# Kernel optimization log

Hardware: AMD Instinct MI355X
Metric: run time of the kernel (lower is better)

## Reference

```python
import jax, jax.numpy as jnp
import numpy as np

LMAX=4; MMAX=2; L2=25; M2=19; C=64; CE=64; NRBF=600; CUT=5.0
HEADS=8; ACH=32; VCH=16; HMSG=64; HFF=128; G=288; NL=2
AVG_NEI=20.0; AVG_NODES=2000.0
N_NODES=2000; N_EDGES=40000; NSPEC=90
# |m| group of each truncated (edge-frame) coefficient, order l=0..4, m=-min(l,2)..min(l,2)
MG = np.array([0, 1,0,1, 2,1,0,1,2, 2,1,0,1,2, 2,1,0,1,2])
# l of each full SH coefficient (25 total)
LOC = np.array([0] + [1]*3 + [2]*5 + [3]*7 + [4]*9)

def silu(x):
    return x * jax.nn.sigmoid(x)

def rms_norm_sh(x, w):
    # x: [N, 25, C]; w: [5, C] per-degree affine weight (rms_norm_sh)
    ms = jnp.mean(x * x, axis=1, keepdims=True)
    return x * jax.lax.rsqrt(ms + 1e-6) * w[LOC][None]

def setup_inputs() -> dict:
    key = jax.random.key(0)
    ks = iter(jax.random.split(key, 64))
    def rn(shape, scale):
        return jax.random.normal(next(ks), shape, dtype=jnp.float32) * scale
    inp = {}
    inp['edge_vectors'] = rn((N_EDGES, 3), 1.5)
    inp['wigner'] = rn((N_EDGES, M2, L2), 0.2)
    inp['wigner_inv'] = rn((N_EDGES, L2, M2), 0.2)
    inp['species_embed'] = rn((NSPEC, C), 1.0)
    inp['edge_species_embed'] = rn((NSPEC, 2 * CE), 1.0)
    DIN = NRBF + 2 * CE  # 728
    inp['deg_W1'] = rn((DIN, 128), DIN ** -0.5)
    inp['deg_b1'] = jnp.zeros((128,), jnp.float32)
    inp['deg_W2'] = rn((128, M2 * C), 128 ** -0.5)
    inp['deg_b2'] = jnp.zeros((M2 * C,), jnp.float32)
    inp['norm1_w'] = jnp.ones((NL, 5, C), jnp.float32)
    inp['rad_W1'] = rn((NL, DIN, 128), DIN ** -0.5)
    inp['rad_b1'] = jnp.zeros((NL, 128), jnp.float32)
    inp['rad_W2'] = rn((NL, 128, 3 * 2 * C), 128 ** -0.5)
    inp['rad_b2'] = jnp.ones((NL, 3 * 2 * C), jnp.float32)
    inp['so2_W'] = rn((NL, 3, 2 * C, HMSG), (2 * C) ** -0.5)
    inp['alpha_W'] = rn((NL, HMSG, HEADS * ACH), HMSG ** -0.5)
    inp['alpha_vec'] = rn((NL, HEADS, ACH), ACH ** -0.5)
    inp['value_W'] = rn((NL, 3, HMSG, HEADS * VCH), HMSG ** -0.5)
    inp['proj_W'] = rn((NL, 3, HEADS * VCH, C), (HEADS * VCH) ** -0.5)
    inp['norm2_w'] = jnp.ones((NL, 5, C), jnp.float32)
    inp['ffn_W1'] = rn((NL, C, HFF), C ** -0.5)
    inp['ffn_b1'] = jnp.zeros((NL, HFF), jnp.float32)
    inp['ffn_W2'] = rn((NL, HFF, C), HFF ** -0.5)
    inp['to_grid'] = rn((G, L2), L2 ** -0.5)
    inp['from_grid'] = rn((L2, G), G ** -0.5)
    inp['final_norm_w'] = jnp.ones((5, C), jnp.float32)
    inp['en_W1'] = rn((C, HFF), C ** -0.5)
    inp['en_b1'] = jnp.zeros((HFF,), jnp.float32)
    inp['en_W2'] = rn((HFF, 1), HFF ** -0.5)
    inp['en_b2'] = jnp.zeros((1,), jnp.float32)
    inp['node_species'] = jax.random.randint(next(ks), (N_NODES,), 0, NSPEC, dtype=jnp.int32)
    inp['senders'] = jax.random.randint(next(ks), (N_EDGES,), 0, N_NODES, dtype=jnp.int32)
    inp['receivers'] = jax.random.randint(next(ks), (N_EDGES,), 0, N_NODES, dtype=jnp.int32)
    inp['n_node'] = jnp.array([N_NODES], jnp.int32)
    return inp

def reference(edge_vectors, wigner, wigner_inv, species_embed, edge_species_embed,
              deg_W1, deg_b1, deg_W2, deg_b2, norm1_w, rad_W1, rad_b1, rad_W2, rad_b2,
              so2_W, alpha_W, alpha_vec, value_W, proj_W, norm2_w, ffn_W1, ffn_b1, ffn_W2,
              to_grid, from_grid, final_norm_w, en_W1, en_b1, en_W2, en_b2,
              node_species, senders, receivers, n_node):
    N = node_species.shape[0]
    E = senders.shape[0]
    mg = jnp.asarray(MG)
    # Gaussian RBF distance expansion (rbf_width=2.0)
    d = jnp.sqrt(jnp.sum(edge_vectors * edge_vectors, axis=-1) + 1e-12)
    offs = jnp.linspace(0.0, CUT, NRBF)
    std = 2.0 * (CUT / (NRBF - 1))
    rbf = jnp.exp(-0.5 * ((d[:, None] - offs[None, :]) / std) ** 2)  # [E, 600]
    # shared atom-edge embedding concat
    ne = edge_species_embed[node_species]
    se, re = jnp.split(ne, 2, axis=-1)
    ee = jnp.concatenate([rbf, se[senders], re[receivers]], axis=1)  # [E, 728]
    # initial node features: species embedding on l=0 component
    x = jnp.zeros((N, L2, C), dtype=edge_vectors.dtype).at[:, 0, :].set(species_embed[node_species])
    # edge degree embedding: radial MLP -> edge-frame coeffs -> rotate back -> scatter
    h = silu(ee @ deg_W1 + deg_b1) @ deg_W2 + deg_b2
    deg = jnp.einsum('elm,emc->elc', wigner_inv, h.reshape(E, M2, C))  # [E,25,C]
    x = x + jax.ops.segment_sum(deg, receivers, num_segments=N) / AVG_NEI
    for i in range(NL):
        # --- SO2 equivariant graph attention ---
        res = x
        xn = rms_norm_sh(x, norm1_w[i])
        msg = jnp.concatenate([xn[senders], xn[receivers]], axis=-1)      # [E,25,2C]
        msg = jnp.einsum('eml,elc->emc', wigner, msg)                     # rotate to edge frame [E,19,2C]
        rad = (silu(ee @ rad_W1[i] + rad_b1[i]) @ rad_W2[i] + rad_b2[i]).reshape(E, MMAX + 1, 2 * C)
        msg = msg * rad[:, mg]                                            # per-|m| radial modulation
        h = jnp.einsum('emc,mco->emo', msg, so2_W[i][mg])                 # SO2 conv [E,19,HMSG]
        a = (silu(h[:, 0, :]) @ alpha_W[i]).reshape(E, HEADS, ACH)        # invariant (m=0) alpha path
        logits = jnp.sum(silu(a) * alpha_vec[i][None], axis=-1)           # [E,HEADS]
        mx = jax.ops.segment_max(logits, receivers, num_segments=N)[receivers]
        ex = jnp.exp(logits - mx)
        den = jax.ops.segment_sum(ex, receivers, num_segments=N)[receivers]
        attn = ex / (den + 1e-12)
        v = jnp.einsum('emo,mov->emv', h, value_W[i][mg]).reshape(E, M2, HEADS, VCH)
        v = (v * attn[:, None, :, None]).reshape(E, M2, HEADS * VCH)
        oe = jnp.einsum('emv,mvc->emc', v, proj_W[i][mg])                 # [E,19,C]
        oe = jnp.einsum('elm,emc->elc', wigner_inv, oe)                   # rotate back [E,25,C]
        x = res + jax.ops.segment_sum(oe, receivers, num_segments=N)
        # --- S2 grid feed-forward ---
        res = x
        xn = rms_norm_sh(x, norm2_w[i])
        g = jnp.einsum('gl,nlc->ngc', to_grid, xn)                        # [N,288,C]
        g = silu(g @ ffn_W1[i] + ffn_b1[i]) @ ffn_W2[i]
        x = res + jnp.einsum('lg,ngc->nlc', from_grid, g)
    # final norm + energy head
    xn = rms_norm_sh(x, final_norm_w)
    g = jnp.einsum('gl,nlc->ngc', to_grid, xn)
    g = silu(g @ en_W1 + en_b1) @ en_W2 + en_b2
    eo = jnp.einsum('lg,ngo->nlo', from_grid, g)
    return eo[:, 0, 0] / AVG_NODES
```

## Files before the change

### kernel.cpp

```cpp
#include <hip/hip_runtime.h>
#include <hip/hip_bf16.h>
#include <math.h>


#define NRBF 600
#define DIN 728
#define GPTS 288
#define CH 8

typedef __attribute__((ext_vector_type(8))) short bf16x8;
typedef __attribute__((ext_vector_type(4))) float f32x4;

__constant__ int d_mg[19] = {0,1,0,1,2,1,0,1,2,2,1,0,1,2,2,1,0,1,2};
__constant__ int d_loc[25] = {0,1,1,1,2,2,2,2,2,3,3,3,3,3,3,3,4,4,4,4,4,4,4,4,4};
__constant__ int d_mg0[5]={0,2,6,11,16};
__constant__ int d_mg1[8]={1,3,5,7,10,12,15,17};
__constant__ int d_mg2[6]={4,8,9,13,14,18};

__device__ inline float silu_f(float v){ return v/(1.0f+__expf(-v)); }
__device__ inline float bf2f(unsigned short u){ return __uint_as_float(((unsigned)u)<<16); }
__device__ inline unsigned short f2bf(float f){
  unsigned b=__float_as_uint(f);
  return (unsigned short)((b + 0x7FFF + ((b>>16)&1)) >> 16);
}

__device__ inline void atomicMaxF(float* addr, float val){
  int* ia=(int*)addr;
  int old=*ia;
  while (__int_as_float(old) < val){
    int assumed=old;
    old = atomicCAS(ia, assumed, __float_as_int(val));
    if (old == assumed) break;
  }
}

__global__ __launch_bounds__(256) void zero_cnt_kernel(int* cnt, int N){
  int i = blockIdx.x*256+threadIdx.x;
  if (i<N) cnt[i]=0;
}
__global__ __launch_bounds__(256) void csr_count_kernel(const int* __restrict__ rcv, int* cnt, int E){
  int i = blockIdx.x*256+threadIdx.x;
  if (i<E) atomicAdd(&cnt[rcv[i]],1);
}
__global__ __launch_bounds__(256) void csr_scan_kernel(const int* __restrict__ cnt,
    int* rowptr, int* fill, int N){
  __shared__ int s_part[256];
  int tid=threadIdx.x;
  int chunk=(N+255)/256;
  int lvals[12];
  int base=tid*chunk;
  int lsum=0;
  for (int i=0;i<chunk && i<12;i++){
    int v=(base+i<N)?cnt[base+i]:0;
    lvals[i]=lsum; lsum+=v;
  }
  s_part[tid]=lsum;
  __syncthreads();
  if (tid==0){
    int run=0;
    for (int t=0;t<256;t++){ int v=s_part[t]; s_part[t]=run; run+=v; }
  }
  __syncthreads();
  int off=s_part[tid];
  for (int i=0;i<chunk && i<12;i++){
    if (base+i<N){ rowptr[base+i]=off+lvals[i]; fill[base+i]=off+lvals[i]; }
  }
  if (tid==255) rowptr[N]=off+lsum;
}
__global__ __launch_bounds__(256) void csr_fill_kernel(const int* __restrict__ rcv,
    int* fill, int* eix, int E){
  int i = blockIdx.x*256+threadIdx.x;
  if (i<E){ int p=atomicAdd(&fill[rcv[i]],1); eix[p]=i; }
}

__global__ __launch_bounds__(256) void wsvb_kernel(const float* __restrict__ so2W,
    const float* __restrict__ valW, unsigned short* __restrict__ wsvb){
  int i=blockIdx.x/3, g=blockIdx.x%3;
  const float* A = so2W + (size_t)i*24576 + g*8192;
  const float* B = valW + (size_t)i*24576 + g*8192;
  unsigned short* C = wsvb + (size_t)blockIdx.x*16384;
  __shared__ float sB[8192];
  for (int j=threadIdx.x;j<2048;j+=256) ((float4*)sB)[j]=((const float4*)B)[j];
  __syncthreads();
  for (int idx=threadIdx.x; idx<16384; idx+=256){
    int k=idx>>7, j=idx&127;
    float acc=0;
    #pragma unroll 4
    for (int o=0;o<64;o++) acc += A[k*64+o]*sB[o*128+j];
    int pos = ((k>>5)*8 + (j>>4))*512 + (((k>>3)&3)*16 + (j&15))*8 + (k&7);
    C[pos]=f2bf(acc);
  }
}

__global__ __launch_bounds__(256) void projb_kernel(const float* __restrict__ pW,
    unsigned short* __restrict__ projb){
  const float* src = pW + (size_t)blockIdx.x*8192;
  unsigned short* dst = projb + (size_t)blockIdx.x*8192;
  for (int idx=threadIdx.x; idx<8192; idx+=256){
    int k=idx>>6, j=idx&63;
    int pos = ((k>>5)*4 + (j>>4))*512 + (((k>>3)&3)*16 + (j&15))*8 + (k&7);
    dst[pos]=f2bf(src[idx]);
  }
}

__global__ __launch_bounds__(256) void packB2g_kernel(const float* __restrict__ src,
    unsigned short* __restrict__ dh, unsigned short* __restrict__ dl, int K, int Nn){
  int ktiles=(K+31)>>5;
  int nnt=Nn>>4;
  int tot=ktiles*nnt*512;
  for (int idx=blockIdx.x*256+threadIdx.x; idx<tot; idx+=gridDim.x*256){
    int f=idx>>9, r=idx&511, lane=r>>3, j=r&7;
    int kt=f/nnt, nt=f-kt*nnt;
    int k=kt*32+(lane>>4)*8+j, c=nt*16+(lane&15);
    float v=(k<K)? src[k*Nn+c] : 0.0f;
    unsigned short h=f2bf(v);
    dh[idx]=h;
    dl[idx]=f2bf(v-bf2f(h));
  }
}

__global__ __launch_bounds__(256) void pack_tg2_kernel(const float* __restrict__ tg,
    unsigned short* __restrict__ tgp){
  int tid=threadIdx.x;
  for (int idx=tid; idx<9216; idx+=256){
    int t=idx>>9, r=idx&511, lane=r>>3, j=r&7;
    int kl=(lane>>4)*8+j, row=t*16+(lane&15);
    float v=(kl<25)? tg[row*25+kl] : 0.0f;
    unsigned short h=f2bf(v);
    tgp[idx]=h;
    tgp[9216+idx]=f2bf(v-bf2f(h));
  }
}

__global__ __launch_bounds__(256) void pack_fg2_kernel(const float* __restrict__ fg,
    unsigned short* __restrict__ fgp){
  int tid=threadIdx.x;
  for (int idx=tid; idx<18432; idx+=256){
    int f=idx>>9, r=idx&511, lane=r>>3, j=r&7;
    int t=f>>1, mt=f&1;
    int row=mt*16+(lane&15), k=(lane>>4)*8+j;
    float v=(row<25 && k<16)? fg[row*288+t*16+k] : 0.0f;
    unsigned short h=f2bf(v);
    fgp[idx]=h;
    fgp[18432+idx]=f2bf(v-bf2f(h));
  }
}

__global__ __launch_bounds__(256) void mlpf_kernel(const float* __restrict__ ev,
    const float* __restrict__ ese, const int* __restrict__ nsp,
    const unsigned short* __restrict__ dw1h, const unsigned short* __restrict__ dw1l,
    const float* __restrict__ db1,
    const unsigned short* __restrict__ dw2h, const unsigned short* __restrict__ dw2l,
    const float* __restrict__ db2,
    const unsigned short* __restrict__ r1h, const unsigned short* __restrict__ r1l,
    const float* __restrict__ rb1,
    const unsigned short* __restrict__ r2h, const unsigned short* __restrict__ r2l,
    const float* __restrict__ rb2,
    const int* __restrict__ snd, const int* __restrict__ rcv, const int* __restrict__ eix,
    int do_deg,
    unsigned short* __restrict__ degout, float* __restrict__ radout, int E){
  int tid=threadIdx.x, wv=tid>>6, lane=tid&63;
  int lanelo=lane&15, khi=lane>>4;
  int p0=blockIdx.x*16;
  __shared__ unsigned short s_eeh[4096], s_eel[4096];
  __shared__ unsigned short s_h1h[2048], s_h1l[2048];
  __shared__ float s_d[16]; __shared__ int s_ss[16], s_rs[16], s_e[16];
  if (tid<16){
    int p=p0+tid;
    int e=(p<E)? eix[p] : -1;
    s_e[tid]=e;
    if (e>=0){
      float vx=ev[3*e], vy=ev[3*e+1], vz=ev[3*e+2];
      s_d[tid]=sqrtf(vx*vx+vy*vy+vz*vz+1e-12f);
      s_ss[tid]=nsp[snd[e]]; s_rs[tid]=nsp[rcv[e]];
    } else { s_d[tid]=0.0f; s_ss[tid]=0; s_rs[tid]=0; }
  }
  __syncthreads();
  const float step=5.0f/599.0f, inv_std=1.0f/(2.0f*step);
  int nta=wv*2, ntb=nta+1;
  f32x4 z4={0,0,0,0};
  f32x4 aD0=z4,aD1=z4,aR0=z4,aR1=z4;
  for (int c=0;c<23;c+=CH){
    int ncur=23-c; if (ncur>CH) ncur=CH;
    for (int idx=tid; idx<ncur*512; idx+=256){
      int f=idx>>9, r=idx&511, ln=r>>3, j=r&7;
      int k=(c+f)*32+((ln>>4)<<3)+j, row=ln&15;
      float v=0.0f;
      if (k<NRBF){ float t=(s_d[row]-k*step)*inv_std; v=__expf(-0.5f*t*t); }
      else if (k<NRBF+64) v=ese[s_ss[row]*128+(k-NRBF)];
      else if (k<DIN)     v=ese[s_rs[row]*128+64+(k-NRBF-64)];
      unsigned short h=f2bf(v);
      s_eeh[idx]=h; s_eel[idx]=f2bf(v-bf2f(h));
    }
    __syncthreads();
    for (int f=0; f<ncur; f++){
      int kt=c+f;
      bf16x8 Ah=*(const bf16x8*)(s_eeh + f*512 + lane*8);
      bf16x8 Al=*(const bf16x8*)(s_eel + f*512 + lane*8);
      size_t ba=(size_t)(kt*8+nta)*512+lane*8;
      {
        bf16x8 Bh=*(const bf16x8*)(r1h+ba), Bl=*(const bf16x8*)(r1l+ba);
        bf16x8 Bh2=*(const bf16x8*)(r1h+ba+512), Bl2=*(const bf16x8*)(r1l+ba+512);
        aR0=__builtin_amdgcn_mfma_f32_16x16x32_bf16(Ah,Bh,aR0,0,0,0);
        aR0=__builtin_amdgcn_mfma_f32_16x16x32_bf16(Al,Bh,aR0,0,0,0);
        aR0=__builtin_amdgcn_mfma_f32_16x16x32_bf16(Ah,Bl,aR0,0,0,0);
        aR1=__builtin_amdgcn_mfma_f32_16x16x32_bf16(Ah,Bh2,aR1,0,0,0);
        aR1=__builtin_amdgcn_mfma_f32_16x16x32_bf16(Al,Bh2,aR1,0,0,0);
        aR1=__builtin_amdgcn_mfma_f32_16x16x32_bf16(Ah,Bl2,aR1,0,0,0);
      }
      if (do_deg){
        bf16x8 Bh=*(const bf16x8*)(dw1h+ba), Bl=*(const bf16x8*)(dw1l+ba);
        bf16x8 Bh2=*(const bf16x8*)(dw1h+ba+512), Bl2=*(const bf16x8*)(dw1l+ba+512);
        aD0=__builtin_amdgcn_mfma_f32_16x16x32_bf16(Ah,Bh,aD0,0,0,0);
        aD0=__builtin_amdgcn_mfma_f32_16x16x32_bf16(Al,Bh,aD0,0,0,0);
        aD0=__builtin_amdgcn_mfma_f32_16x16x32_bf16(Ah,Bl,aD0,0,0,0);
        aD1=__builtin_amdgcn_mfma_f32_16x16x32_bf16(Ah,Bh2,aD1,0,0,0);
        aD1=__builtin_amdgcn_mfma_f32_16x16x32_bf16(Al,Bh2,aD1,0,0,0);
        aD1=__builtin_amdgcn_mfma_f32_16x16x32_bf16(Ah,Bl2,aD1,0,0,0);
      }
    }
    __syncthreads();
  }
  int nmlp = do_deg ? 2 : 1;
  #pragma unroll 1
  for (int it=0; it<nmlp; it++){
    int is_deg = (it==1);
    f32x4 a0 = is_deg ? aD0 : aR0;
    f32x4 a1 = is_deg ? aD1 : aR1;
    const float* b1 = is_deg ? db1 : rb1;
    #pragma unroll
    for (int q=0;q<4;q++){
      int row=khi*4+q;
      {
        int col=nta*16+lanelo;
        float v=silu_f(a0[q]+b1[col]);
        int pos=row*128 + (((col>>3)^(row&7))<<3) + (col&7);
        unsigned short h=f2bf(v);
        s_h1h[pos]=h; s_h1l[pos]=f2bf(v-bf2f(h));
      }
      {
        int col=ntb*16+lanelo;
        float v=silu_f(a1[q]+b1[col]);
        int pos=row*128 + (((col>>3)^(row&7))<<3) + (col&7);
        unsigned short h=f2bf(v);
        s_h1h[pos]=h; s_h1l[pos]=f2bf(v-bf2f(h));
      }
    }
    __syncthreads();
    bf16x8 Ahh[4],Ahl[4];
    #pragma unroll
    for (int kt=0;kt<4;kt++){
      int o=lanelo*128 + (((kt*4+khi)^(lanelo&7))<<3);
      Ahh[kt]=*(const bf16x8*)(s_h1h+o);
      Ahl[kt]=*(const bf16x8*)(s_h1l+o);
    }
    __syncthreads();
    if (is_deg){
      for (int nt=wv; nt<76; nt+=4){
        f32x4 acc=z4;
        #pragma unroll
        for (int kt=0;kt<4;kt++){
          size_t bo=(size_t)(kt*76+nt)*512+lane*8;
          bf16x8 Bh=*(const bf16x8*)(dw2h+bo), Bl=*(const bf16x8*)(dw2l+bo);
          acc=__builtin_amdgcn_mfma_f32_16x16x32_bf16(Ahh[kt],Bh,acc,0,0,0);
          acc=__builtin_amdgcn_mfma_f32_16x16x32_bf16(Ahl[kt],Bh,acc,0,0,0);
          acc=__builtin_amdgcn_mfma_f32_16x16x32_bf16(Ahh[kt],Bl,acc,0,0,0);
        }
        int col=nt*16+lanelo;
        float bb=db2[col];
        #pragma unroll
        for (int q=0;q<4;q++){
          int p=p0+khi*4+q;
          if (p<E) degout[(size_t)p*1216+col]=f2bf(acc[q]+bb);
        }
      }
    } else {
      for (int nt=wv; nt<24; nt+=4){
        f32x4 acc=z4;
        #pragma unroll
        for (int kt=0;kt<4;kt++){
          size_t bo=(size_t)(kt*24+nt)*512+lane*8;
          bf16x8 Bh=*(const bf16x8*)(r2h+bo), Bl=*(const bf16x8*)(r2l+bo);
          acc=__builtin_amdgcn_mfma_f32_16x16x32_bf16(Ahh[kt],Bh,acc,0,0,0);
          acc=__builtin_amdgcn_mfma_f32_16x16x32_bf16(Ahl[kt],Bh,acc,0,0,0);
          acc=__builtin_amdgcn_mfma_f32_16x16x32_bf16(Ahh[kt],Bl,acc,0,0,0);
        }
        int col=nt*16+lanelo;
        float bb=rb2[col];
        #pragma unroll
        for (int q=0;q<4;q++){
          int e=s_e[khi*4+q];
          if (e>=0) radout[(size_t)e*384+col]=acc[q]+bb;
        }
      }
    }
  }
}

__global__ __launch_bounds__(256) void node_sum_kernel(const unsigned short* __restrict__ msgb,
    const float* __restrict__ winv, const int* __restrict__ rowptr, const int* __restrict__ eix,
    const int* __restrict__ nsp, const float* __restrict__ spe,
    float* __restrict__ x, int mode, int N){
  int n=blockIdx.x, tid=threadIdx.x, wv=tid>>6, lane=tid&63;
  __shared__ float s_winv[4][480];
  __shared__ unsigned short s_oe[4][1216];
  __shared__ float4 s_red[4][400];
  int row0=rowptr[n];
  int cnt=rowptr[n+1]-row0;
  float4 acc[7];
  #pragma unroll
  for (int t=0;t<7;t++) acc[t]=make_float4(0,0,0,0);
  for (int j=wv; j<cnt; j+=4){
    int p=row0+j;
    int e=eix[p];
    asm volatile("s_waitcnt lgkmcnt(0)" ::: "memory");
    for (int k=lane;k<475;k+=64) s_winv[wv][k]=winv[(size_t)e*475+k];
    if (mode==1){
      for (int k=lane;k<152;k+=64)
        ((int4*)s_oe[wv])[k]=*(const int4*)(msgb+(size_t)p*1216+k*8);
    } else {
      for (int k=lane;k<152;k+=64){
        int m=k>>3, jj=k&7;
        ((int4*)s_oe[wv])[k]=*(const int4*)(msgb+(size_t)p*2432+m*128+jj*8);
      }
    }
    asm volatile("s_waitcnt lgkmcnt(0)" ::: "memory");
    const unsigned* o2=(const unsigned*)s_oe[wv];
    #pragma unroll
    for (int t=0;t<7;t++){
      int sI=lane+t*64;
      if (sI<400){
        int l=sI>>4, c4=sI&15;
        const float* wr=s_winv[wv]+l*19;
        float4 a=acc[t];
        #pragma unroll
        for (int m=0;m<19;m++){
          float w=wr[m];
          unsigned ua=o2[m*32+c4*2], ub=o2[m*32+c4*2+1];
          a.x+=w*bf2f((unsigned short)(ua&0xffffu));
          a.y+=w*bf2f((unsigned short)(ua>>16));
          a.z+=w*bf2f((unsigned short)(ub&0xffffu));
          a.w+=w*bf2f((unsigned short)(ub>>16));
        }
        acc[t]=a;
      }
    }
  }
  asm volatile("s_waitcnt lgkmcnt(0)" ::: "memory");
  #pragma unroll
  for (int t=0;t<7;t++){
    int sI=lane+t*64;
    if (sI<400) s_red[wv][sI]=acc[t];
  }
  __syncthreads();
  float4* xp=(float4*)(x+(size_t)n*1600);
  if (mode==0){
    for (int j=tid;j<400;j+=256){
      float4 a=s_red[0][j], b=s_red[1][j], c=s_red[2][j], d=s_red[3][j];
      float4 cur=xp[j];
      cur.x+=a.x+b.x+c.x+d.x;
      cur.y+=a.y+b.y+c.y+d.y;
      cur.z+=a.z+b.z+c.z+d.z;
      cur.w+=a.w+b.w+c.w+d.w;
      xp[j]=cur;
    }
  } else {
    int sp=nsp[n];
    const float4* sp4=(const float4*)(spe+(size_t)sp*64);
    for (int j=tid;j<400;j+=256){
      int l=j>>4, c4=j&15;
      float4 a=s_red[0][j], b=s_red[1][j], c=s_red[2][j], d=s_red[3][j];
      float4 base=(l==0)? sp4[c4] : make_float4(0,0,0,0);
      float4 o;
      o.x=base.x+0.05f*(a.x+b.x+c.x+d.x);
      o.y=base.y+0.05f*(a.y+b.y+c.y+d.y);
      o.z=base.z+0.05f*(a.z+b.z+c.z+d.z);
      o.w=base.w+0.05f*(a.w+b.w+c.w+d.w);
      xp[j]=o;
    }
  }
}

__global__ __launch_bounds__(256) void rmsnorm_kernel(const float* __restrict__ x,
    const float* __restrict__ w, float* __restrict__ xn, int N){
  int n = blockIdx.x, tid = threadIdx.x;
  __shared__ float s_x[1600];
  __shared__ float s_part[256];
  __shared__ float s_ms[64];
  const float* xr = x + (size_t)n*1600;
  for (int j=tid;j<1600;j+=256) s_x[j]=xr[j];
  __syncthreads();
  {
    int c = tid&63, seg = tid>>6;
    float acc=0;
    for (int l=seg;l<25;l+=4){ float v=s_x[l*64+c]; acc+=v*v; }
    s_part[tid]=acc;
  }
  __syncthreads();
  if (tid<64){
    float m=(s_part[tid]+s_part[tid+64]+s_part[tid+128]+s_part[tid+192])*(1.0f/25.0f);
    s_ms[tid]=rsqrtf(m+1e-6f);
  }
  __syncthreads();
  float* xo = xn + (size_t)n*1600;
  for (int j=tid;j<1600;j+=256){
    int l=j>>6, c=j&63;
    xo[j]=s_x[j]*s_ms[c]*w[d_loc[l]*64+c];
  }
}

__global__ __launch_bounds__(256) void init_mxden_kernel(float* mx, float* den, int N){
  int idx = blockIdx.x*256+threadIdx.x;
  if (idx < N*8){ mx[idx]=-3.0e38f; den[idx]=0.0f; }
}

__global__ __launch_bounds__(256) void logits_kernel(const float* __restrict__ xn,
    const float* __restrict__ wig, const float* __restrict__ radb,
    const float* __restrict__ so2W, const float* __restrict__ alphaW, const float* __restrict__ alphaV,
    const int* __restrict__ snd, const int* __restrict__ rcv,
    float* __restrict__ logits, float* __restrict__ mx, int E){
  int e = blockIdx.x, tid = threadIdx.x;
  __shared__ float s_cat[3200];
  __shared__ float s_wig0[25];
  __shared__ float s_msg0[128];
  __shared__ float s_sh0[64];
  __shared__ float s_a[256];
  int s = snd[e], r = rcv[e];
  const float4* xs4 = (const float4*)(xn + (size_t)s*1600);
  const float4* xr4 = (const float4*)(xn + (size_t)r*1600);
  float4* cat4 = (float4*)s_cat;
  for (int j=tid;j<400;j+=256){
    int l=j>>4, c4=j&15;
    cat4[l*32+c4]    = xs4[j];
    cat4[l*32+16+c4] = xr4[j];
  }
  if (tid<25) s_wig0[tid]=wig[(size_t)e*475+tid];
  __syncthreads();
  if (tid<128){
    float acc=0;
    #pragma unroll
    for (int l=0;l<25;l++) acc += s_wig0[l]*s_cat[l*128+tid];
    s_msg0[tid]=acc*radb[(size_t)e*384+tid];
  }
  __syncthreads();
  if (tid<64){
    float acc=0;
    #pragma unroll
    for (int k=0;k<128;k++) acc += s_msg0[k]*so2W[k*64+tid];
    s_sh0[tid]=silu_f(acc);
  }
  __syncthreads();
  {
    float acc=0;
    #pragma unroll
    for (int o=0;o<64;o++) acc += s_sh0[o]*alphaW[o*256+tid];
    s_a[tid]=silu_f(acc)*alphaV[tid];
  }
  __syncthreads();
  if (tid<8){
    float lg=0;
    #pragma unroll
    for (int q=0;q<32;q++) lg += s_a[tid*32+q];
    logits[(size_t)e*8+tid]=lg;
    atomicMaxF(&mx[r*8+tid], lg);
  }
}

__global__ __launch_bounds__(256) void den_kernel(const float* __restrict__ logits,
    const float* __restrict__ mx, const int* __restrict__ rcv,
    float* __restrict__ den, int E){
  int idx = blockIdx.x*256+threadIdx.x;
  if (idx >= E*8) return;
  int e = idx>>3, hd = idx&7, r = rcv[e];
  atomicAdd(&den[r*8+hd], __expf(logits[idx]-mx[r*8+hd]));
}

__global__ __launch_bounds__(256) void msg_kernel(const float* __restrict__ xn,
    const float* __restrict__ wig, const float* __restrict__ radb,
    const int* __restrict__ snd, const int* __restrict__ rcv, const int* __restrict__ eix,
    unsigned short* __restrict__ msgb, int E){
  __shared__ float s_wig[1900];
  int tid=threadIdx.x, wv=tid>>6, lane=tid&63;
  int p=blockIdx.x*4+wv;
  bool act=(p<E);
  int pc=act? p : (E-1);
  int e=eix[pc];
  int node=(lane<32)? snd[e] : rcv[e];
  int c2=(lane&31)*2;
  int col0=c2+((lane>>5)<<6);
  const float* xb=xn+(size_t)node*1600+c2;
  float ca[25], cb[25];
  #pragma unroll
  for (int l=0;l<25;l++){
    float2 v=*(const float2*)(xb+l*64);
    ca[l]=v.x; cb[l]=v.y;
  }
  float* swig=s_wig+wv*475;
  for (int j=lane;j<475;j+=64) swig[j]=wig[(size_t)e*475+j];
  float ra0,ra1,rb0,rb1,rc0,rc1;
  {
    const float* rb_=radb+(size_t)e*384;
    float2 v0=*(const float2*)(rb_+col0);
    float2 v1=*(const float2*)(rb_+128+col0);
    float2 v2=*(const float2*)(rb_+256+col0);
    ra0=v0.x; ra1=v0.y; rb0=v1.x; rb1=v1.y; rc0=v2.x; rc1=v2.y;
  }
  __syncthreads();
  unsigned short* dst=msgb+(size_t)pc*2432+col0;
  constexpr int mgc[19]={0,1,0,1,2,1,0,1,2,2,1,0,1,2,2,1,0,1,2};
  if (act){
    #pragma unroll
    for (int m=0;m<19;m++){
      float a0=0.0f,a1=0.0f;
      const float* wr=swig+m*25;
      #pragma unroll
      for (int l=0;l<25;l++){ float w=wr[l]; a0+=w*ca[l]; a1+=w*cb[l]; }
      float r0,r1;
      if (mgc[m]==0){ r0=ra0; r1=ra1; }
      else if (mgc[m]==1){ r0=rb0; r1=rb1; }
      else { r0=rc0; r1=rc1; }
      a0*=r0; a1*=r1;
      unsigned packv=((unsigned)f2bf(a1)<<16)|(unsigned)f2bf(a0);
      *(unsigned*)(dst+m*128)=packv;
    }
  }
}

__global__ __launch_bounds__(256) void attn_gemm_kernel(unsigned short* __restrict__ msgb,
    const unsigned short* __restrict__ wsvp, const unsigned short* __restrict__ projp,
    const float* __restrict__ logits, const float* __restrict__ mx, const float* __restrict__ den,
    const int* __restrict__ eix, const int* __restrict__ rcv, int E){
  int tid=threadIdx.x, wv=tid>>6, lane=tid&63;
  int lanelo=lane&15, khi=lane>>4;
  int p0=blockIdx.x*16;
  __shared__ unsigned short s_vv[2176];
  __shared__ float s_attn[16][8];
  __shared__ short s_r2e[304], s_r2m[304];
  for (int j=tid;j<304;j+=256){
    int e,m;
    if (j<80){ e=j/5; m=d_mg0[j%5]; }
    else if (j<208){ int q=j-80; e=q>>3; m=d_mg1[q&7]; }
    else { int q=j-208; e=q/6; m=d_mg2[q%6]; }
    s_r2e[j]=(short)e; s_r2m[j]=(short)m;
  }
  if (tid<128){
    int i=tid>>3, h=tid&7, p=p0+i;
    float a=0.0f;
    if (p<E){
      int e=eix[p]; int r=rcv[e];
      a=__expf(logits[(size_t)e*8+h]-mx[r*8+h])/(den[r*8+h]+1e-12f);
    }
    s_attn[i][h]=a;
  }
  __syncthreads();
  const int4* wp4=(const int4*)wsvp;
  const int4* pp4=(const int4*)projp;
  for (int t=0;t<19;t++){
    int g=(t<5)?0:((t<13)?1:2);
    int R=t*16+lanelo;
    int ei=s_r2e[R], mi=s_r2m[R];
    int pp=p0+ei;
    size_t abase=((size_t)((pp<E)?pp:0))*2432 + (size_t)mi*128;
    bf16x8 A[4];
    #pragma unroll
    for (int kt=0;kt<4;kt++)
      A[kt]=*(const bf16x8*)(msgb + abase + kt*32 + khi*8);
    #pragma unroll
    for (int h2=0;h2<2;h2++){
      int nt=wv*2+h2;
      f32x4 acc={0,0,0,0};
      #pragma unroll
      for (int kt=0;kt<4;kt++){
        int4 tt=wp4[g*2048+(kt*8+nt)*64+lane];
        acc=__builtin_amdgcn_mfma_f32_16x16x32_bf16(A[kt],*(bf16x8*)&tt,acc,0,0,0);
      }
      int col=nt*16+lanelo;
      #pragma unroll
      for (int q=0;q<4;q++){
        int r16=khi*4+q;
        int ei2=s_r2e[t*16+r16];
        s_vv[r16*136+col]=f2bf(acc[q]*s_attn[ei2][nt]);
      }
    }
    __syncthreads();
    {
      bf16x8 A2[4];
      #pragma unroll
      for (int kt=0;kt<4;kt++)
        A2[kt]=*(const bf16x8*)(s_vv + lanelo*136 + kt*32 + khi*8);
      f32x4 acc={0,0,0,0};
      #pragma unroll
      for (int kt=0;kt<4;kt++){
        int4 tt=pp4[g*1024+(kt*4+wv)*64+lane];
        acc=__builtin_amdgcn_mfma_f32_16x16x32_bf16(A2[kt],*(bf16x8*)&tt,acc,0,0,0);
      }
      int col=wv*16+lanelo;
      #pragma unroll
      for (int q=0;q<4;q++){
        int R2=t*16+khi*4+q;
        int pi=p0+s_r2e[R2];
        if (pi<E) msgb[(size_t)pi*2432 + (size_t)s_r2m[R2]*128 + col]=f2bf(acc[q]);
      }
    }
    __syncthreads();
  }
}

__global__ __launch_bounds__(256) void grid_ffn_mfma_kernel(const float* __restrict__ xn,
    const unsigned short* __restrict__ tgp, const unsigned short* __restrict__ fgp,
    const unsigned short* __restrict__ w1p, const unsigned short* __restrict__ w2p,
    const float* __restrict__ b1, float* __restrict__ x, int N){
  int n=blockIdx.x, tid=threadIdx.x, wv=tid>>6, lane=tid&63;
  int lanelo=lane&15, khi=lane>>4;
  __shared__ __align__(16) char s_mem[74240];
  unsigned short* s_w1=(unsigned short*)s_mem;
  unsigned short* s_xn=(unsigned short*)(s_mem+32768);
  float* s_b1=(float*)(s_mem+40960);
  unsigned short* scr=(unsigned short*)(s_mem+41472)+(size_t)wv*4096;
  for (int j=tid;j<2048;j+=256) ((int4*)s_w1)[j]=((const int4*)w1p)[j];
  if (tid<128) s_b1[tid]=b1[tid];
  { int4 z={0,0,0,0}; for (int j=tid;j<512;j+=256) ((int4*)s_xn)[j]=z; }
  __syncthreads();
  {
    const float* xr=xn+(size_t)n*1600;
    for (int j=tid;j<1600;j+=256){
      int k=j>>6, c=j&63;
      float v=xr[j];
      unsigned short h=f2bf(v);
      s_xn[c*32+k]=h;
      s_xn[2048+c*32+k]=f2bf(v-bf2f(h));
    }
  }
  __syncthreads();
  bf16x8 XBh[4],XBl[4];
  #pragma unroll
  for (int ct=0;ct<4;ct++){
    int o=(ct*16+lanelo)*32 + khi*8;
    XBh[ct]=*(const bf16x8*)(s_xn+o);
    XBl[ct]=*(const bf16x8*)(s_xn+2048+o);
  }
  f32x4 oacc[2][4];
  #pragma unroll
  for (int mt=0;mt<2;mt++)
    #pragma unroll
    for (int nt=0;nt<4;nt++){ f32x4 z={0,0,0,0}; oacc[mt][nt]=z; }
  for (int t=wv;t<18;t+=4){
    bf16x8 Atgh=*(const bf16x8*)(tgp + t*512 + lane*8);
    bf16x8 Atgl=*(const bf16x8*)(tgp + 9216 + t*512 + lane*8);
    #pragma unroll
    for (int ct=0;ct<4;ct++){
      f32x4 g={0,0,0,0};
      g=__builtin_amdgcn_mfma_f32_16x16x32_bf16(Atgh,XBh[ct],g,0,0,0);
      g=__builtin_amdgcn_mfma_f32_16x16x32_bf16(Atgl,XBh[ct],g,0,0,0);
      g=__builtin_amdgcn_mfma_f32_16x16x32_bf16(Atgh,XBl[ct],g,0,0,0);
      #pragma unroll
      for (int q=0;q<4;q++){
        int row=khi*4+q, col=ct*16+lanelo;
        int pos=row*64 + (((col>>3)^(row&7))<<3) + (col&7);
        float v=g[q]; unsigned short h=f2bf(v);
        scr[pos]=h; scr[1024+pos]=f2bf(v-bf2f(h));
      }
    }
    bf16x8 Agh[2],Agl[2];
    #pragma unroll
    for (int kt=0;kt<2;kt++){
      int o=lanelo*64 + (((kt*4+khi)^(lanelo&7))<<3);
      Agh[kt]=*(const bf16x8*)(scr+o);
      Agl[kt]=*(const bf16x8*)(scr+1024+o);
    }
    #pragma unroll
    for (int nt=0;nt<8;nt++){
      f32x4 h={0,0,0,0};
      #pragma unroll
      for (int kt=0;kt<2;kt++){
        bf16x8 Bh=*(const bf16x8*)(s_w1 + (kt*8+nt)*512 + lane*8);
        bf16x8 Bl=*(const bf16x8*)(s_w1 + 8192 + (kt*8+nt)*512 + lane*8);
        h=__builtin_amdgcn_mfma_f32_16x16x32_bf16(Agh[kt],Bh,h,0,0,0);
        h=__builtin_amdgcn_mfma_f32_16x16x32_bf16(Agl[kt],Bh,h,0,0,0);
        h=__builtin_amdgcn_mfma_f32_16x16x32_bf16(Agh[kt],Bl,h,0,0,0);
      }
      #pragma unroll
      for (int q=0;q<4;q++){
        int row=khi*4+q, col=nt*16+lanelo;
        float v=silu_f(h[q]+s_b1[col]);
        int pos=row*128 + (((col>>3)^(row&7))<<3) + (col&7);
        unsigned short hh=f2bf(v);
        scr[pos]=hh; scr[2048+pos]=f2bf(v-bf2f(hh));
      }
    }
    bf16x8 Ahh[4],Ahl[4];
    #pragma unroll
    for (int kt=0;kt<4;kt++){
      int o=lanelo*128 + (((kt*4+khi)^(lanelo&7))<<3);
      Ahh[kt]=*(const bf16x8*)(scr+o);
      Ahl[kt]=*(const bf16x8*)(scr+2048+o);
    }
    #pragma unroll
    for (int nt=0;nt<4;nt++){
      f32x4 o4={0,0,0,0};
      #pragma unroll
      for (int kt=0;kt<4;kt++){
        bf16x8 Bh=*(const bf16x8*)(w2p + (kt*4+nt)*512 + lane*8);
        bf16x8 Bl=*(const bf16x8*)(w2p + 8192 + (kt*4+nt)*512 + lane*8);
        o4=__builtin_amdgcn_mfma_f32_16x16x32_bf16(Ahh[kt],Bh,o4,0,0,0);
        o4=__builtin_amdgcn_mfma_f32_16x16x32_bf16(Ahl[kt],Bh,o4,0,0,0);
        o4=__builtin_amdgcn_mfma_f32_16x16x32_bf16(Ahh[kt],Bl,o4,0,0,0);
      }
      #pragma unroll
      for (int q=0;q<4;q++){
        int ch=nt*16+lanelo, rowk=khi*4+q;
        int pos=ch*32 + (((rowk>>3)^(ch&3))<<3) + (rowk&7);
        float v=o4[q]; unsigned short hh=f2bf(v);
        scr[pos]=hh; scr[2048+pos]=f2bf(v-bf2f(hh));
      }
    }
    bf16x8 Boh[4],Bol[4];
    #pragma unroll
    for (int nt=0;nt<4;nt++){
      int ch=nt*16+lanelo;
      int o=ch*32 + ((khi^(ch&3))<<3);
      Boh[nt]=*(const bf16x8*)(scr+o);
      Bol[nt]=*(const bf16x8*)(scr+2048+o);
    }
    #pragma unroll
    for (int mt=0;mt<2;mt++){
      bf16x8 Afh=*(const bf16x8*)(fgp + (t*2+mt)*512 + lane*8);
      bf16x8 Afl=*(const bf16x8*)(fgp + 18432 + (t*2+mt)*512 + lane*8);
      #pragma unroll
      for (int nt=0;nt<4;nt++){
        oacc[mt][nt]=__builtin_amdgcn_mfma_f32_16x16x32_bf16(Afh,Boh[nt],oacc[mt][nt],0,0,0);
        oacc[mt][nt]=__builtin_amdgcn_mfma_f32_16x16x32_bf16(Afl,Boh[nt],oacc[mt][nt],0,0,0);
        oacc[mt][nt]=__builtin_amdgcn_mfma_f32_16x16x32_bf16(Afh,Bol[nt],oacc[mt][nt],0,0,0);
      }
    }
  }
  __syncthreads();
  float* pout=(float*)s_mem;
  #pragma unroll
  for (int mt=0;mt<2;mt++)
    #pragma unroll
    for (int nt=0;nt<4;nt++)
      #pragma unroll
      for (int q=0;q<4;q++){
        int row=mt*16+khi*4+q, col=nt*16+lanelo;
        pout[wv*2048 + row*64 + col]=oacc[mt][nt][q];
      }
  __syncthreads();
  for (int j=tid;j<1600;j+=256)
    x[(size_t)n*1600+j] += pout[j]+pout[2048+j]+pout[4096+j]+pout[6144+j];
}

__global__ __launch_bounds__(256) void energy_mfma_kernel(const float* __restrict__ xn,
    const unsigned short* __restrict__ tgp, const float* __restrict__ fg,
    const unsigned short* __restrict__ enw1p, const float* __restrict__ b1,
    const float* __restrict__ w2, const float* __restrict__ b2,
    float* __restrict__ out, int N){
  int n=blockIdx.x, tid=threadIdx.x, wv=tid>>6, lane=tid&63;
  int lanelo=lane&15, khi=lane>>4;
  __shared__ __align__(16) char s_mem[59584];
  unsigned short* s_w1=(unsigned short*)s_mem;
  unsigned short* s_xn=(unsigned short*)(s_mem+32768);
  float* s_b1=(float*)(s_mem+40960);
  float* s_w2=(float*)(s_mem+41472);
  float* s_fg0=(float*)(s_mem+41984);
  float* s_red=(float*)(s_mem+43136);
  unsigned short* scr=(unsigned short*)(s_mem+43200)+(size_t)wv*2048;
  for (int j=tid;j<2048;j+=256) ((int4*)s_w1)[j]=((const int4*)enw1p)[j];
  if (tid<128){ s_b1[tid]=b1[tid]; s_w2[tid]=w2[tid]; }
  for (int j=tid;j<288;j+=256) s_fg0[j]=fg[j];
  { int4 z={0,0,0,0}; for (int j=tid;j<512;j+=256) ((int4*)s_xn)[j]=z; }
  __syncthreads();
  {
    const float* xr=xn+(size_t)n*1600;
    for (int j=tid;j<1600;j+=256){
      int k=j>>6, c=j&63;
      float v=xr[j];
      unsigned short h=f2bf(v);
      s_xn[c*32+k]=h;
      s_xn[2048+c*32+k]=f2bf(v-bf2f(h));
    }
  }
  __syncthreads();
  bf16x8 XBh[4],XBl[4];
  #pragma unroll
  for (int ct=0;ct<4;ct++){
    int o=(ct*16+lanelo)*32 + khi*8;
    XBh[ct]=*(const bf16x8*)(s_xn+o);
    XBl[ct]=*(const bf16x8*)(s_xn+2048+o);
  }
  float b2v=b2[0];
  float e=0.0f;
  for (int t=wv;t<18;t+=4){
    bf16x8 Atgh=*(const bf16x8*)(tgp + t*512 + lane*8);
    bf16x8 Atgl=*(const bf16x8*)(tgp + 9216 + t*512 + lane*8);
    #pragma unroll
    for (int ct=0;ct<4;ct++){
      f32x4 g={0,0,0,0};
      g=__builtin_amdgcn_mfma_f32_16x16x32_bf16(Atgh,XBh[ct],g,0,0,0);
      g=__builtin_amdgcn_mfma_f32_16x16x32_bf16(Atgl,XBh[ct],g,0,0,0);
      g=__builtin_amdgcn_mfma_f32_16x16x32_bf16(Atgh,XBl[ct],g,0,0,0);
      #pragma unroll
      for (int q=0;q<4;q++){
        int row=khi*4+q, col=ct*16+lanelo;
        int pos=row*64 + (((col>>3)^(row&7))<<3) + (col&7);
        float v=g[q]; unsigned short h=f2bf(v);
        scr[pos]=h; scr[1024+pos]=f2bf(v-bf2f(h));
      }
    }
    bf16x8 Agh[2],Agl[2];
    #pragma unroll
    for (int kt=0;kt<2;kt++){
      int o=lanelo*64 + (((kt*4+khi)^(lanelo&7))<<3);
      Agh[kt]=*(const bf16x8*)(scr+o);
      Agl[kt]=*(const bf16x8*)(scr+1024+o);
    }
    #pragma unroll
    for (int nt=0;nt<8;nt++){
      f32x4 h={0,0,0,0};
      #pragma unroll
      for (int kt=0;kt<2;kt++){
        bf16x8 Bh=*(const bf16x8*)(s_w1 + (kt*8+nt)*512 + lane*8);
        bf16x8 Bl=*(const bf16x8*)(s_w1 + 8192 + (kt*8+nt)*512 + lane*8);
        h=__builtin_amdgcn_mfma_f32_16x16x32_bf16(Agh[kt],Bh,h,0,0,0);
        h=__builtin_amdgcn_mfma_f32_16x16x32_bf16(Agl[kt],Bh,h,0,0,0);
        h=__builtin_amdgcn_mfma_f32_16x16x32_bf16(Agh[kt],Bl,h,0,0,0);
      }
      #pragma unroll
      for (int q=0;q<4;q++){
        int row=khi*4+q, col=nt*16+lanelo;
        float v=silu_f(h[q]+s_b1[col]);
        e += v*s_w2[col]*s_fg0[t*16+row];
      }
    }
    if (lanelo==0){
      #pragma unroll
      for (int q=0;q<4;q++) e += s_fg0[t*16+khi*4+q]*b2v;
    }
  }
  #pragma unroll
  for (int d=1;d<64;d<<=1) e += __shfl_xor(e,d);
  if (lane==0) s_red[wv]=e;
  __syncthreads();
  if (tid==0) out[n]=(s_red[0]+s_red[1]+s_red[2]+s_red[3])*(1.0f/2000.0f);
}

extern "C" void kernel_launch(void* const* d_in, const int* in_sizes, int n_in,
                              void* d_out, int out_size, void* d_ws, size_t ws_size,
                              hipStream_t stream){
  (void)n_in; (void)out_size; (void)ws_size;
  const float* ev   = (const float*)d_in[0];
  const float* wig  = (const float*)d_in[1];
  const float* winv = (const float*)d_in[2];
  const float* spe  = (const float*)d_in[3];
  const float* ese  = (const float*)d_in[4];
  const float* degW1= (const float*)d_in[5];
  const float* degb1= (const float*)d_in[6];
  const float* degW2= (const float*)d_in[7];
  const float* degb2= (const float*)d_in[8];
  const float* n1w  = (const float*)d_in[9];
  const float* radW1= (const float*)d_in[10];
  const float* radb1= (const float*)d_in[11];
  const float* radW2= (const float*)d_in[12];
  const float* radb2= (const float*)d_in[13];
  const float* so2W = (const float*)d_in[14];
  const float* aW   = (const float*)d_in[15];
  const float* aV   = (const float*)d_in[16];
  const float* vW   = (const float*)d_in[17];
  const float* pW   = (const float*)d_in[18];
  const float* n2w  = (const float*)d_in[19];
  const float* fW1  = (const float*)d_in[20];
  const float* fb1  = (const float*)d_in[21];
  const float* fW2  = (const float*)d_in[22];
  const float* tg   = (const float*)d_in[23];
  const float* fg   = (const float*)d_in[24];
  const float* fnw  = (const float*)d_in[25];
  const float* enW1 = (const float*)d_in[26];
  const float* enb1 = (const float*)d_in[27];
  const float* enW2 = (const float*)d_in[28];
  const float* enb2 = (const float*)d_in[29];
  const int* nsp = (const int*)d_in[30];
  const int* snd = (const int*)d_in[31];
  const int* rcv = (const int*)d_in[32];
  int N = in_sizes[30];
  int E = in_sizes[31];
  float* out = (float*)d_out;

  float* ws = (float*)d_ws;
  size_t off = 0;
  float* radbuf = ws + off; off += (size_t)E*384;
  float* logits = ws + off; off += (size_t)E*8;
  float* mx     = ws + off; off += (size_t)N*8;
  float* den    = ws + off; off += (size_t)N*8;
  float* x      = ws + off; off += (size_t)N*1600;
  float* xn     = ws + off; off += (size_t)N*1600;
  unsigned short* wsvb  = (unsigned short*)(ws + off); off += (size_t)6*16384/2;
  unsigned short* projb = (unsigned short*)(ws + off); off += (size_t)6*8192/2;
  int* cnt      = (int*)(ws + off); off += (size_t)N;
  int* rowptr   = (int*)(ws + off); off += (size_t)(N+1);
  int* fill     = (int*)(ws + off); off += (size_t)N;
  int* eixbuf   = (int*)(ws + off); off += (size_t)E;
  off = (off + 3) & ~((size_t)3);
  unsigned short* msgb  = (unsigned short*)(ws + off); off += (size_t)E*1216;
  unsigned short* tgp   = (unsigned short*)(ws + off); off += 9216;
  unsigned short* fgp   = (unsigned short*)(ws + off); off += 18432;
  unsigned short* wwp   = (unsigned short*)(ws + off); off += 32768;
  unsigned short* enw1p = (unsigned short*)(ws + off); off += 8192;
  unsigned short* degw1p = (unsigned short*)(ws + off); off += 94208;
  unsigned short* degw2p = (unsigned short*)(ws + off); off += 155648;
  unsigned short* radw1p = (unsigned short*)(ws + off); off += 94208*2;
  unsigned short* radw2p = (unsigned short*)(ws + off); off += 49152*2;

  zero_cnt_kernel<<<(N+255)/256, 256, 0, stream>>>(cnt, N);
  csr_count_kernel<<<(E+255)/256, 256, 0, stream>>>(rcv, cnt, E);
  csr_scan_kernel<<<1, 256, 0, stream>>>(cnt, rowptr, fill, N);
  csr_fill_kernel<<<(E+255)/256, 256, 0, stream>>>(rcv, fill, eixbuf, E);
  wsvb_kernel<<<6, 256, 0, stream>>>(so2W, vW, wsvb);
  projb_kernel<<<6, 256, 0, stream>>>(pW, projb);
  pack_tg2_kernel<<<1, 256, 0, stream>>>(tg, tgp);
  pack_fg2_kernel<<<1, 256, 0, stream>>>(fg, fgp);
  for (int i=0;i<2;i++){
    unsigned short* wl = wwp + (size_t)i*32768;
    packB2g_kernel<<<8, 256, 0, stream>>>(fW1 + (size_t)i*8192, wl, wl+8192, 64, 128);
    packB2g_kernel<<<8, 256, 0, stream>>>(fW2 + (size_t)i*8192, wl+16384, wl+24576, 128, 64);
  }
  packB2g_kernel<<<8, 256, 0, stream>>>(enW1, enw1p, enw1p+8192, 64, 128);
  packB2g_kernel<<<32, 256, 0, stream>>>(degW1, degw1p, degw1p+94208, DIN, 128);
  packB2g_kernel<<<32, 256, 0, stream>>>(degW2, degw2p, degw2p+155648, 128, 1216);
  for (int i=0;i<2;i++){
    unsigned short* r1 = radw1p + (size_t)i*188416;
    unsigned short* r2 = radw2p + (size_t)i*98304;
    packB2g_kernel<<<32, 256, 0, stream>>>(radW1 + (size_t)i*DIN*128, r1, r1+94208, DIN, 128);
    packB2g_kernel<<<16, 256, 0, stream>>>(radW2 + (size_t)i*128*384, r2, r2+49152, 128, 384);
  }

  mlpf_kernel<<<(E+15)/16, 256, 0, stream>>>(ev, ese, nsp,
      degw1p, degw1p+94208, degb1, degw2p, degw2p+155648, degb2,
      radw1p, radw1p+94208, radb1,
      radw2p, radw2p+49152, radb2,
      snd, rcv, eixbuf, 1, msgb, radbuf, E);
  node_sum_kernel<<<N, 256, 0, stream>>>(msgb, winv, rowptr, eixbuf, nsp, spe, x, 1, N);

  for (int i=0;i<2;i++){
    if (i==1){
      unsigned short* r1 = radw1p + (size_t)188416;
      unsigned short* r2 = radw2p + (size_t)98304;
      mlpf_kernel<<<(E+15)/16, 256, 0, stream>>>(ev, ese, nsp,
          degw1p, degw1p+94208, degb1, degw2p, degw2p+155648, degb2,
          r1, r1+94208, radb1+128,
          r2, r2+49152, radb2+384,
          snd, rcv, eixbuf, 0, msgb, radbuf, E);
    }
    rmsnorm_kernel<<<N, 256, 0, stream>>>(x, n1w + (size_t)i*320, xn, N);
    init_mxden_kernel<<<(N*8+255)/256, 256, 0, stream>>>(mx, den, N);
    logits_kernel<<<E, 256, 0, stream>>>(xn, wig, radbuf, so2W + (size_t)i*24576,
                                         aW + (size_t)i*64*256, aV + (size_t)i*256,
                                         snd, rcv, logits, mx, E);
    den_kernel<<<(E*8+255)/256, 256, 0, stream>>>(logits, mx, rcv, den, E);
    msg_kernel<<<(E+3)/4, 256, 0, stream>>>(xn, wig, radbuf, snd, rcv, eixbuf, msgb, E);
    attn_gemm_kernel<<<(E+15)/16, 256, 0, stream>>>(msgb,
                                                    wsvb + (size_t)i*3*16384, projb + (size_t)i*3*8192,
                                                    logits, mx, den, eixbuf, rcv, E);
    node_sum_kernel<<<N, 256, 0, stream>>>(msgb, winv, rowptr, eixbuf, nsp, spe, x, 0, N);
    rmsnorm_kernel<<<N, 256, 0, stream>>>(x, n2w + (size_t)i*320, xn, N);
    grid_ffn_mfma_kernel<<<N, 256, 0, stream>>>(xn, tgp, fgp,
                                                wwp + (size_t)i*32768, wwp + (size_t)i*32768 + 16384,
                                                fb1 + (size_t)i*128, x, N);
  }
  rmsnorm_kernel<<<N, 256, 0, stream>>>(x, fnw, xn, N);
  energy_mfma_kernel<<<N, 256, 0, stream>>>(xn, tgp, fg, enw1p, enb1, enW2, enb2, out, N);
}
```

Before: 2.790 ms.

## Fuse attention logit computation into message rotation kernel

Removes the separate per-edge logits kernel, which used one block per edge and re-read both endpoint feature rows. Logits are now computed inside the message kernel, one wave per edge, reusing the m=0 rotated message already in registers. The so2 and alpha projections run per wave through shared memory, and only wave-local LDS waits are used instead of block barriers. This saves a launch and a redundant gather of node features, at the cost of more per-wave work and weight reads inside the message kernel.

```diff
diff --git a/kernel.cpp b/kernel.cpp
--- a/kernel.cpp
+++ b/kernel.cpp
@@ -414,58 +414,6 @@
   if (idx < N*8){ mx[idx]=-3.0e38f; den[idx]=0.0f; }
 }
 
-__global__ __launch_bounds__(256) void logits_kernel(const float* __restrict__ xn,
-    const float* __restrict__ wig, const float* __restrict__ radb,
-    const float* __restrict__ so2W, const float* __restrict__ alphaW, const float* __restrict__ alphaV,
-    const int* __restrict__ snd, const int* __restrict__ rcv,
-    float* __restrict__ logits, float* __restrict__ mx, int E){
-  int e = blockIdx.x, tid = threadIdx.x;
-  __shared__ float s_cat[3200];
-  __shared__ float s_wig0[25];
-  __shared__ float s_msg0[128];
-  __shared__ float s_sh0[64];
-  __shared__ float s_a[256];
-  int s = snd[e], r = rcv[e];
-  const float4* xs4 = (const float4*)(xn + (size_t)s*1600);
-  const float4* xr4 = (const float4*)(xn + (size_t)r*1600);
-  float4* cat4 = (float4*)s_cat;
-  for (int j=tid;j<400;j+=256){
-    int l=j>>4, c4=j&15;
-    cat4[l*32+c4]    = xs4[j];
-    cat4[l*32+16+c4] = xr4[j];
-  }
-  if (tid<25) s_wig0[tid]=wig[(size_t)e*475+tid];
-  __syncthreads();
-  if (tid<128){
-    float acc=0;
-    #pragma unroll
-    for (int l=0;l<25;l++) acc += s_wig0[l]*s_cat[l*128+tid];
-    s_msg0[tid]=acc*radb[(size_t)e*384+tid];
-  }
-  __syncthreads();
-  if (tid<64){
-    float acc=0;
-    #pragma unroll
-    for (int k=0;k<128;k++) acc += s_msg0[k]*so2W[k*64+tid];
-    s_sh0[tid]=silu_f(acc);
-  }
-  __syncthreads();
-  {
-    float acc=0;
-    #pragma unroll
-    for (int o=0;o<64;o++) acc += s_sh0[o]*alphaW[o*256+tid];
-    s_a[tid]=silu_f(acc)*alphaV[tid];
-  }
-  __syncthreads();
-  if (tid<8){
-    float lg=0;
-    #pragma unroll
-    for (int q=0;q<32;q++) lg += s_a[tid*32+q];
-    logits[(size_t)e*8+tid]=lg;
-    atomicMaxF(&mx[r*8+tid], lg);
-  }
-}
-
 __global__ __launch_bounds__(256) void den_kernel(const float* __restrict__ logits,
     const float* __restrict__ mx, const int* __restrict__ rcv,
     float* __restrict__ den, int E){
@@ -477,9 +425,12 @@
 
 __global__ __launch_bounds__(256) void msg_kernel(const float* __restrict__ xn,
     const float* __restrict__ wig, const float* __restrict__ radb,
+    const float* __restrict__ so2W, const float* __restrict__ alphaW, const float* __restrict__ alphaV,
     const int* __restrict__ snd, const int* __restrict__ rcv, const int* __restrict__ eix,
-    unsigned short* __restrict__ msgb, int E){
+    unsigned short* __restrict__ msgb, float* __restrict__ logits, float* __restrict__ mx, int E){
   __shared__ float s_wig[1900];
+  __shared__ float s_m0[4][128];
+  __shared__ float s_sh0[4][64];
   int tid=threadIdx.x, wv=tid>>6, lane=tid&63;
   int p=blockIdx.x*4+wv;
   bool act=(p<E);
@@ -508,6 +459,7 @@
   __syncthreads();
   unsigned short* dst=msgb+(size_t)pc*2432+col0;
   constexpr int mgc[19]={0,1,0,1,2,1,0,1,2,2,1,0,1,2,2,1,0,1,2};
+  float m0a=0.0f, m0b=0.0f;
   if (act){
     #pragma unroll
     for (int m=0;m<19;m++){
@@ -520,8 +472,42 @@
       else if (mgc[m]==1){ r0=rb0; r1=rb1; }
       else { r0=rc0; r1=rc1; }
       a0*=r0; a1*=r1;
+      if (m==0){ m0a=a0; m0b=a1; }
       unsigned packv=((unsigned)f2bf(a1)<<16)|(unsigned)f2bf(a0);
       *(unsigned*)(dst+m*128)=packv;
+    }
+  }
+  s_m0[wv][col0]=m0a; s_m0[wv][col0+1]=m0b;
+  asm volatile("s_waitcnt lgkmcnt(0)" ::: "memory");
+  {
+    const float* m0p=s_m0[wv];
+    float accs=0.0f;
+    #pragma unroll 8
+    for (int k=0;k<128;k++) accs += m0p[k]*so2W[k*64+lane];
+    s_sh0[wv][lane]=silu_f(accs);
+  }
+  asm volatile("s_waitcnt lgkmcnt(0)" ::: "memory");
+  {
+    const float* sh=s_sh0[wv];
+    int j0=lane*4;
+    float4 av=*(const float4*)(alphaV+j0);
+    float4 aacc={0,0,0,0};
+    #pragma unroll 8
+    for (int o=0;o<64;o++){
+      float s=sh[o];
+      float4 w=*(const float4*)(alphaW+o*256+j0);
+      aacc.x+=s*w.x; aacc.y+=s*w.y; aacc.z+=s*w.z; aacc.w+=s*w.w;
+    }
+    float part = silu_f(aacc.x)*av.x + silu_f(aacc.y)*av.y
+               + silu_f(aacc.z)*av.z + silu_f(aacc.w)*av.w;
+    part += __shfl_xor(part,1);
+    part += __shfl_xor(part,2);
+    part += __shfl_xor(part,4);
+    if (act && (lane&7)==0){
+      int h=lane>>3;
+      int r=rcv[e];
+      logits[(size_t)e*8+h]=part;
+      atomicMaxF(&mx[r*8+h], part);
     }
   }
 }
@@ -952,11 +938,11 @@
     }
     rmsnorm_kernel<<<N, 256, 0, stream>>>(x, n1w + (size_t)i*320, xn, N);
     init_mxden_kernel<<<(N*8+255)/256, 256, 0, stream>>>(mx, den, N);
-    logits_kernel<<<E, 256, 0, stream>>>(xn, wig, radbuf, so2W + (size_t)i*24576,
-                                         aW + (size_t)i*64*256, aV + (size_t)i*256,
-                                         snd, rcv, logits, mx, E);
+    msg_kernel<<<(E+3)/4, 256, 0, stream>>>(xn, wig, radbuf,
+                                            so2W + (size_t)i*24576,
+                                            aW + (size_t)i*64*256, aV + (size_t)i*256,
+                                            snd, rcv, eixbuf, msgb, logits, mx, E);
     den_kernel<<<(E*8+255)/256, 256, 0, stream>>>(logits, mx, rcv, den, E);
-    msg_kernel<<<(E+3)/4, 256, 0, stream>>>(xn, wig, radbuf, snd, rcv, eixbuf, msgb, E);
     attn_gemm_kernel<<<(E+15)/16, 256, 0, stream>>>(msgb,
                                                     wsvb + (size_t)i*3*16384, projb + (size_t)i*3*8192,
                                                     logits, mx, den, eixbuf, rcv, E);
```

Result: faster. 2.726 ms (-2.3%).
